# Performance work log

Hardware: AMD Instinct MI355X
Metric: run time of the kernel (lower is better)

Reference implementation:

```python
import jax, jax.numpy as jnp
import numpy as np

B, HH, WW, C = 16, 56, 56, 384
HEADS, WS, SHIFT, HID = 12, 7, 3, 1536
N = WS * WS
EPS = 1e-5


def _rel_pos_index(ws):
    coords = np.stack(np.meshgrid(np.arange(ws), np.arange(ws), indexing='ij'))  # (2, ws, ws)
    cf = coords.reshape(2, -1)
    rel = (cf[:, :, None] - cf[:, None, :]).transpose(1, 2, 0).copy()  # (N, N, 2)
    rel[:, :, 0] += ws - 1
    rel[:, :, 1] += ws - 1
    rel[:, :, 0] *= 2 * ws - 1
    return rel.sum(-1)  # (N, N) int


def _attn_mask(H, W, ws, shift):
    img = np.zeros((H, W))
    sl = (slice(0, -ws), slice(-ws, -shift), slice(-shift, None))
    cnt = 0
    for h in sl:
        for w in sl:
            img[h, w] = cnt
            cnt += 1
    mw = img.reshape(H // ws, ws, W // ws, ws).transpose(0, 2, 1, 3).reshape(-1, ws * ws)  # (nW, N)
    am = mw[:, None, :] - mw[:, :, None]
    return np.where(am != 0, -100.0, 0.0).astype(np.float32)  # (nW, N, N)

REL_IDX = jnp.asarray(_rel_pos_index(WS))
ATTN_MASK = jnp.asarray(_attn_mask(HH, WW, WS, SHIFT))


def _ln(x, w, b):
    m = x.mean(-1, keepdims=True)
    v = ((x - m) ** 2).mean(-1, keepdims=True)
    return (x - m) * jax.lax.rsqrt(v + EPS) * w + b


def _win_part(x, ws):
    b, h, w, c = x.shape
    x = x.reshape(b, h // ws, ws, w // ws, ws, c).transpose(0, 1, 3, 2, 4, 5)
    return x.reshape(-1, ws * ws, c)


def _win_rev(wins, ws, h, w):
    c = wins.shape[-1]
    b = wins.shape[0] // ((h // ws) * (w // ws))
    x = wins.reshape(b, h // ws, w // ws, ws, ws, c).transpose(0, 1, 3, 2, 4, 5)
    return x.reshape(b, h, w, c)


def setup_inputs() -> dict:
    key = jax.random.key(0)
    ks = jax.random.split(key, 12)
    s = lambda fan: 1.0 / np.sqrt(fan)
    return {
        'x': jax.random.normal(ks[0], (B, HH * WW, C), jnp.float32),
        'norm1_w': jnp.ones((C,), jnp.float32),
        'norm1_b': jnp.zeros((C,), jnp.float32),
        'qkv_w': jax.random.normal(ks[1], (3 * C, C), jnp.float32) * s(C),
        'qkv_b': jnp.zeros((3 * C,), jnp.float32),
        'bias_table': jax.random.normal(ks[2], ((2 * WS - 1) ** 2, HEADS), jnp.float32) * 0.02,
        'proj_w': jax.random.normal(ks[3], (C, C), jnp.float32) * s(C),
        'proj_b': jnp.zeros((C,), jnp.float32),
        'norm2_w': jnp.ones((C,), jnp.float32),
        'norm2_b': jnp.zeros((C,), jnp.float32),
        'mlp_w1': jax.random.normal(ks[4], (HID, C), jnp.float32) * s(C),
        'mlp_b1': jnp.zeros((HID,), jnp.float32),
        'mlp_w2': jax.random.normal(ks[5], (C, HID), jnp.float32) * s(HID),
        'mlp_b2': jnp.zeros((C,), jnp.float32),
        'H': HH,
        'W': WW,
    }


def reference(x, norm1_w, norm1_b, qkv_w, qkv_b, bias_table, proj_w, proj_b,
              norm2_w, norm2_b, mlp_w1, mlp_b1, mlp_w2, mlp_b2, H, W):
    b = x.shape[0]
    shortcut = x
    h = _ln(x, norm1_w, norm1_b).reshape(b, H, W, C)
    # cyclic shift (H, W divisible by WS -> no padding needed)
    h = jnp.roll(h, shift=(-SHIFT, -SHIFT), axis=(1, 2))
    xw = _win_part(h, WS)  # (b*nW, N, C)
    Bw = xw.shape[0]
    hd = C // HEADS
    qkv = xw @ qkv_w.T + qkv_b  # (Bw, N, 3C)
    qkv = qkv.reshape(Bw, N, 3, HEADS, hd).transpose(2, 0, 3, 1, 4)
    q, k, v = qkv[0], qkv[1], qkv[2]  # (Bw, heads, N, hd)
    attn = jnp.einsum('bhnd,bhmd->bhnm', q * (hd ** -0.5), k)
    rel_bias = bias_table[REL_IDX.reshape(-1)].reshape(N, N, HEADS).transpose(2, 0, 1)
    attn = attn + rel_bias[None]
    nW = ATTN_MASK.shape[0]
    attn = attn.reshape(Bw // nW, nW, HEADS, N, N) + ATTN_MASK[None, :, None]
    attn = jax.nn.softmax(attn.reshape(Bw, HEADS, N, N), axis=-1)
    out = jnp.einsum('bhnm,bhmd->bhnd', attn, v).transpose(0, 2, 1, 3).reshape(Bw, N, C)
    out = out @ proj_w.T + proj_b
    h = _win_rev(out, WS, H, W)
    h = jnp.roll(h, shift=(SHIFT, SHIFT), axis=(1, 2)).reshape(b, H * W, C)
    x = shortcut + h
    y = _ln(x, norm2_w, norm2_b)
    y = jax.nn.gelu(y @ mlp_w1.T + mlp_b1, approximate=False) @ mlp_w2.T + mlp_b2
    return x + y
```

## Files before the change

### kernel.cpp

```cpp
#include <hip/hip_runtime.h>

typedef unsigned short ushort_t;
typedef __attribute__((ext_vector_type(8))) short bf16x8;
typedef __attribute__((ext_vector_type(4))) float f32x4;

__device__ __forceinline__ float b2f(ushort_t u) {
    union { float f; unsigned int u32; } x; x.u32 = ((unsigned int)u) << 16; return x.f;
}
__device__ __forceinline__ ushort_t f2b(float f) {
    union { float f; unsigned int u; } x; x.f = f;
    unsigned int r = x.u + 0x7fffu + ((x.u >> 16) & 1u);
    return (ushort_t)(r >> 16);
}
__device__ __forceinline__ float ldin(const void* p, size_t i, int fp32) {
    return fp32 ? ((const float*)p)[i] : b2f(((const ushort_t*)p)[i]);
}
__device__ __forceinline__ void gl_lds16(const ushort_t* g, ushort_t* l) {
    __builtin_amdgcn_global_load_lds((const __attribute__((address_space(1))) unsigned int*)g,
                                     (__attribute__((address_space(3))) unsigned int*)l, 16, 0, 0);
}
__device__ __forceinline__ float gelu_f(float x) {
    float xx = x * x;
    float u  = x * (0.7978845608028654f + 0.0356774081363f * xx);
    float a  = __builtin_fabsf(u);
    float e2 = __expf(-2.0f * a);
    float t  = (1.0f - e2) * __builtin_amdgcn_rcpf(1.0f + e2);
    t = __builtin_copysignf(t, u);
    return 0.5f * x * (1.0f + t);
}

struct Cv { const void* s; ushort_t* d; int n; };
struct CvA { Cv a[13]; };
__global__ void convert_all(CvA c, int total) {
    int fp32 = (*(const unsigned int*)c.a[0].s == 0x3F800000u);
    for (int idx = blockIdx.x * blockDim.x + threadIdx.x; idx < total; idx += gridDim.x * blockDim.x) {
        int i = idx, k = 0;
        while (k < 12 && i >= c.a[k].n) { i -= c.a[k].n; ++k; }
        c.a[k].d[i] = fp32 ? f2b(((const float*)c.a[k].s)[i]) : ((const ushort_t*)c.a[k].s)[i];
    }
}

__global__ __launch_bounds__(256) void ln_kernel(const void* __restrict__ x,
                                                 const ushort_t* __restrict__ w,
                                                 const ushort_t* __restrict__ bvec,
                                                 ushort_t* __restrict__ out, int mode, int row_base,
                                                 const void* __restrict__ flagsrc)
{
    int wave = threadIdx.x >> 6, lane = threadIdx.x & 63;
    int lr = blockIdx.x * 4 + wave;
    int r = row_base + lr;
    int f32 = (mode == 1) ? 1 : (*(const unsigned int*)flagsrc == 0x3F800000u);
    long src;
    if (mode == 0) {
        int win = r / 49, pos = r % 49;
        int b = win >> 6, wy = (win >> 3) & 7, wx = win & 7;
        int py = pos / 7, px = pos - py * 7;
        int ys = wy * 7 + py + 3; if (ys >= 56) ys -= 56;
        int xs = wx * 7 + px + 3; if (xs >= 56) xs -= 56;
        src = (long)b * 3136 + ys * 56 + xs;
    } else {
        src = r;
    }
    float v[6];
    float s = 0.f, sq = 0.f;
#pragma unroll
    for (int j = 0; j < 6; ++j) {
        v[j] = ldin(x, src * 384 + lane + 64 * j, f32);
        s += v[j]; sq += v[j] * v[j];
    }
#pragma unroll
    for (int off = 32; off; off >>= 1) { s += __shfl_xor(s, off); sq += __shfl_xor(sq, off); }
    float mean = s * (1.f / 384.f);
    float var  = sq * (1.f / 384.f) - mean * mean;
    float rstd = rsqrtf(var + 1e-5f);
    ushort_t* op = out + (size_t)lr * 384;
#pragma unroll
    for (int j = 0; j < 6; ++j) {
        int c = lane + 64 * j;
        op[c] = f2b((v[j] - mean) * rstd * b2f(w[c]) + b2f(bvec[c]));
    }
}

__global__ __launch_bounds__(256) void attn_mfma(const ushort_t* __restrict__ qkv,
                                                 const ushort_t* __restrict__ bt,
                                                 ushort_t* __restrict__ out)
{
    __shared__ __align__(16) ushort_t Pb[4][64 * 72];
    __shared__ __align__(16) ushort_t Vb[4][32 * 72];
    int win = blockIdx.x;
    int t = threadIdx.x;
    int wave = t >> 6, lane = t & 63;
    int quad = lane >> 4, l16 = lane & 15;
    ushort_t* P  = Pb[wave];
    ushort_t* VT = Vb[wave];
    int wimg = win & 63;
    int wy = wimg >> 3, wx = wimg & 7;
    const float scale = 0.17677669529663687f;

    int rjv[4], cjv[4], gjv[4], cvalid[4];
#pragma unroll
    for (int jt = 0; jt < 4; ++jt) {
        int c = jt * 16 + l16;
        cvalid[jt] = (c < 49);
        int rj = c / 7, cj = c - rj * 7;
        rjv[jt] = rj; cjv[jt] = cj;
        int gjy = (wy == 7) ? (rj < 4 ? 1 : 2) : 0;
        int gjx = (wx == 7) ? (cj < 4 ? 1 : 2) : 0;
        gjv[jt] = gjy * 3 + gjx;
    }

    for (int hh = 0; hh < 3; ++hh) {
        int head = wave * 3 + hh;
        size_t base = (size_t)win * 49 * 1152 + (size_t)head * 32;

        bf16x8 qf[4], kf[4];
#pragma unroll
        for (int i = 0; i < 4; ++i) {
            int row = i * 16 + l16;
            bf16x8 z = {};
            qf[i] = z; kf[i] = z;
            if (row < 49) {
                qf[i] = *(const bf16x8*)(qkv + base + (size_t)row * 1152 + quad * 8);
                kf[i] = *(const bf16x8*)(qkv + base + (size_t)row * 1152 + 384 + quad * 8);
            }
        }
#pragma unroll
        for (int e = 0; e < 4; ++e) {
            int j = e * 16 + (lane >> 2);
            int db = (lane & 3) * 8;
            ushort_t buf[8] = {};
            if (j < 49) *(uint4*)buf = *(const uint4*)(qkv + base + (size_t)j * 1152 + 768 + db);
#pragma unroll
            for (int s = 0; s < 8; ++s) VT[(db + s) * 72 + j] = buf[s];
        }

        f32x4 Sv[4][4];
#pragma unroll
        for (int i = 0; i < 4; ++i)
#pragma unroll
            for (int j = 0; j < 4; ++j) {
                f32x4 z = {};
                Sv[i][j] = __builtin_amdgcn_mfma_f32_16x16x32_bf16(qf[i], kf[j], z, 0, 0, 0);
            }

#pragma unroll
        for (int it = 0; it < 4; ++it) {
#pragma unroll
            for (int r = 0; r < 4; ++r) {
                int m = it * 16 + quad * 4 + r;
                int ri = m / 7, ci = m - ri * 7;
                int giy = (wy == 7) ? (ri < 4 ? 1 : 2) : 0;
                int gix = (wx == 7) ? (ci < 4 ? 1 : 2) : 0;
                int gi = giy * 3 + gix;
                float vals[4];
                float vmax = -1e30f;
#pragma unroll
                for (int jt = 0; jt < 4; ++jt) {
                    float sv = -1e30f;
                    if (m < 49 && cvalid[jt]) {
                        int rel = (ri - rjv[jt] + 6) * 13 + (ci - cjv[jt] + 6);
                        sv = Sv[it][jt][r] * scale + b2f(bt[rel * 12 + head]);
                        if (gi != gjv[jt]) sv -= 100.f;
                    }
                    vals[jt] = sv;
                    vmax = fmaxf(vmax, sv);
                }
#pragma unroll
                for (int off = 1; off < 16; off <<= 1) vmax = fmaxf(vmax, __shfl_xor(vmax, off));
                float ssum = 0.f;
#pragma unroll
                for (int jt = 0; jt < 4; ++jt) { float e = __expf(vals[jt] - vmax); vals[jt] = e; ssum += e; }
#pragma unroll
                for (int off = 1; off < 16; off <<= 1) ssum += __shfl_xor(ssum, off);
                float inv = __builtin_amdgcn_rcpf(ssum);
#pragma unroll
                for (int jt = 0; jt < 4; ++jt) P[m * 72 + jt * 16 + l16] = f2b(vals[jt] * inv);
            }
        }

        f32x4 Ov[4][2] = {};
#pragma unroll
        for (int kk = 0; kk < 2; ++kk) {
            bf16x8 vb[2];
            vb[0] = *(const bf16x8*)&VT[(l16) * 72 + kk * 32 + quad * 8];
            vb[1] = *(const bf16x8*)&VT[(16 + l16) * 72 + kk * 32 + quad * 8];
#pragma unroll
            for (int mt = 0; mt < 4; ++mt) {
                bf16x8 pa = *(const bf16x8*)&P[(mt * 16 + l16) * 72 + kk * 32 + quad * 8];
                Ov[mt][0] = __builtin_amdgcn_mfma_f32_16x16x32_bf16(pa, vb[0], Ov[mt][0], 0, 0, 0);
                Ov[mt][1] = __builtin_amdgcn_mfma_f32_16x16x32_bf16(pa, vb[1], Ov[mt][1], 0, 0, 0);
            }
        }
#pragma unroll
        for (int mt = 0; mt < 4; ++mt)
#pragma unroll
            for (int r = 0; r < 4; ++r) {
                int m = mt * 16 + quad * 4 + r;
                if (m < 49) {
                    size_t orow = ((size_t)win * 49 + m) * 384 + (size_t)head * 32;
                    out[orow + l16]      = f2b(Ov[mt][0][r]);
                    out[orow + 16 + l16] = f2b(Ov[mt][1][r]);
                }
            }
    }
}

template <int EPI>
__global__ __launch_bounds__(512, 4) void gemm_k(const ushort_t* __restrict__ A,
                                                 const ushort_t* __restrict__ Bw,
                                                 const ushort_t* __restrict__ bias,
                                                 const void* __restrict__ residv,
                                                 void* __restrict__ outv,
                                                 int N, int K, int Mp, long rbase,
                                                 const void* __restrict__ flagsrc)
{
    __shared__ __align__(16) ushort_t lA[3][256 * 32];
    __shared__ __align__(16) ushort_t lB[3][128 * 32];

    unsigned gx = gridDim.x;
    unsigned nwg = gx * gridDim.y;
    unsigned lid = blockIdx.y * gx + blockIdx.x;
    unsigned xcd = lid & 7u, chunk_i = lid >> 3;
    unsigned q = nwg >> 3, r8 = nwg & 7u;
    unsigned logical = (xcd < r8 ? xcd * (q + 1) : r8 * (q + 1) + (xcd - r8) * q) + chunk_i;
    int m0 = (int)(logical / gx) * 256, n0 = (int)(logical % gx) * 128;

    int t = threadIdx.x;
    int wave = t >> 6, lane = t & 63;
    int quad = lane >> 4, l16 = lane & 15;
    int wrow = (wave >> 1) * 64, wcol = (wave & 1) * 64;
    f32x4 acc[4][4] = {};

    float bb[4];
#pragma unroll
    for (int j = 0; j < 4; ++j) bb[j] = b2f(bias[n0 + wcol + j * 16 + l16]);
    asm volatile("" :: "v"(bb[0]), "v"(bb[1]), "v"(bb[2]), "v"(bb[3]));

    const ushort_t* gp[3];
    ushort_t* lp[3];
    int lstr[3];
#pragma unroll
    for (int e = 0; e < 3; ++e) {
        int chunk = wave * 3 + e;
        int a = (chunk < 16);
        int trow = (a ? chunk * 16 : (chunk - 16) * 16) + (lane >> 2);
        int fsw = (trow >> 1) & 3;
        int scol = ((lane & 3) ^ fsw) * 8;
        int grow = a ? (m0 + trow) : (n0 + trow);
        if (a && grow >= Mp) grow = Mp - 1;
        gp[e] = (a ? A : Bw) + (size_t)grow * K + scol;
        lp[e] = a ? &lA[0][chunk * 512] : &lB[0][(chunk - 16) * 512];
        lstr[e] = a ? 256 * 32 : 128 * 32;
    }

    auto stage = [&](int buf, int k0) {
#pragma unroll
        for (int e = 0; e < 3; ++e)
            gl_lds16(gp[e] + k0, lp[e] + buf * lstr[e]);
    };

    int sl = (quad ^ ((l16 >> 1) & 3)) * 8;
    auto compute = [&](int buf) {
        bf16x8 af[4], bf[4];
#pragma unroll
        for (int i = 0; i < 4; ++i)
            af[i] = *(const bf16x8*)(&lA[buf][(wrow + i * 16 + l16) * 32 + sl]);
#pragma unroll
        for (int j = 0; j < 4; ++j)
            bf[j] = *(const bf16x8*)(&lB[buf][(wcol + j * 16 + l16) * 32 + sl]);
#pragma unroll
        for (int i = 0; i < 4; ++i)
#pragma unroll
            for (int j = 0; j < 4; ++j)
                acc[i][j] = __builtin_amdgcn_mfma_f32_16x16x32_bf16(af[i], bf[j], acc[i][j], 0, 0, 0);
    };

    int T = K >> 5;
    stage(0, 0);
    stage(1, 32);

    int cur = 0;
    for (int tt = 0; tt < T - 1; ++tt) {
        asm volatile("s_waitcnt vmcnt(3)" ::: "memory");
        __builtin_amdgcn_s_barrier();
        if (tt + 2 < T) stage(cur == 0 ? 2 : cur - 1, (tt + 2) * 32);
        compute(cur);
        cur = (cur == 2) ? 0 : cur + 1;
    }
    asm volatile("s_waitcnt vmcnt(0)" ::: "memory");
    __builtin_amdgcn_s_barrier();
    compute(cur);

    int rf32 = (EPI == 2) ? (*(const unsigned int*)flagsrc == 0x3F800000u) : 1;

#pragma unroll
    for (int i = 0; i < 4; ++i) {
#pragma unroll
        for (int rix = 0; rix < 4; ++rix) {
            int m = m0 + wrow + i * 16 + quad * 4 + rix;
            if (m >= Mp) continue;
            unsigned orow = 0;
            if (EPI == 2) {
                int mg = (int)rbase + m;
                int win = mg / 49, pos = mg - win * 49;
                int b = win >> 6, wy = (win >> 3) & 7, wx = win & 7;
                int py = pos / 7, px = pos - py * 7;
                int y = wy * 7 + py + 3; if (y >= 56) y -= 56;
                int x = wx * 7 + px + 3; if (x >= 56) x -= 56;
                orow = (unsigned)(b * 3136 + y * 56 + x);
            } else if (EPI == 3) {
                orow = (unsigned)(rbase + m);
            }
#pragma unroll
            for (int j = 0; j < 4; ++j) {
                int n = n0 + wcol + j * 16 + l16;
                float vv = acc[i][j][rix] + bb[j];
                if (EPI == 0) {
                    ((ushort_t*)outv)[(unsigned)m * (unsigned)N + (unsigned)n] = f2b(vv);
                } else if (EPI == 1) {
                    ((ushort_t*)outv)[(unsigned)m * (unsigned)N + (unsigned)n] = f2b(gelu_f(vv));
                } else {
                    float r = ldin(residv, (size_t)orow * 384 + n, rf32);
                    ((float*)outv)[(size_t)orow * 384 + n] = vv + r;
                }
            }
        }
    }
}

extern "C" void kernel_launch(void* const* d_in, const int* in_sizes, int n_in,
                              void* d_out, int out_size, void* d_ws, size_t ws_size,
                              hipStream_t stream)
{
    (void)in_sizes; (void)n_in; (void)out_size;
    char* ws = (char*)d_ws;
    size_t off = 0;
    auto alloc = [&](size_t bytes) { size_t p = off; off = (off + bytes + 255) & ~(size_t)255; return p; };

    size_t o_n1w  = alloc(384 * 2);
    size_t o_n1b  = alloc(384 * 2);
    size_t o_qw   = alloc(442368ull * 2);
    size_t o_qb   = alloc(1152 * 2);
    size_t o_bt   = alloc(2028 * 2);
    size_t o_pw   = alloc(147456ull * 2);
    size_t o_pb   = alloc(384 * 2);
    size_t o_n2w  = alloc(384 * 2);
    size_t o_n2b  = alloc(384 * 2);
    size_t o_w1   = alloc(589824ull * 2);
    size_t o_b1   = alloc(1536 * 2);
    size_t o_w2   = alloc(589824ull * 2);
    size_t o_b2   = alloc(384 * 2);

    size_t avail = (ws_size > off) ? ws_size - off : 0;
    int M_c;
    if      (avail >= (size_t)50176 * 3840 + 1024) M_c = 50176;
    else if (avail >= (size_t)12544 * 3840 + 1024) M_c = 12544;
    else                                            M_c = 6272;
    int nch = 50176 / M_c;
    size_t o_s1 = alloc((size_t)M_c * 768);
    size_t o_s2 = alloc((size_t)M_c * 3072);

    ushort_t* n1w  = (ushort_t*)(ws + o_n1w);
    ushort_t* n1b  = (ushort_t*)(ws + o_n1b);
    ushort_t* qw   = (ushort_t*)(ws + o_qw);
    ushort_t* qb   = (ushort_t*)(ws + o_qb);
    ushort_t* bt   = (ushort_t*)(ws + o_bt);
    ushort_t* pw   = (ushort_t*)(ws + o_pw);
    ushort_t* pb   = (ushort_t*)(ws + o_pb);
    ushort_t* n2w  = (ushort_t*)(ws + o_n2w);
    ushort_t* n2b  = (ushort_t*)(ws + o_n2b);
    ushort_t* w1   = (ushort_t*)(ws + o_w1);
    ushort_t* b1   = (ushort_t*)(ws + o_b1);
    ushort_t* w2   = (ushort_t*)(ws + o_w2);
    ushort_t* b2v  = (ushort_t*)(ws + o_b2);
    ushort_t* s1   = (ushort_t*)(ws + o_s1);
    ushort_t* s2   = (ushort_t*)(ws + o_s2);
    const void* x  = d_in[0];
    const void* fs = d_in[1];
    float* xmid    = (float*)d_out;

    CvA ca;
    ca.a[0]  = {d_in[1],  n1w, 384};
    ca.a[1]  = {d_in[2],  n1b, 384};
    ca.a[2]  = {d_in[3],  qw,  442368};
    ca.a[3]  = {d_in[4],  qb,  1152};
    ca.a[4]  = {d_in[5],  bt,  2028};
    ca.a[5]  = {d_in[6],  pw,  147456};
    ca.a[6]  = {d_in[7],  pb,  384};
    ca.a[7]  = {d_in[8],  n2w, 384};
    ca.a[8]  = {d_in[9],  n2b, 384};
    ca.a[9]  = {d_in[10], w1,  589824};
    ca.a[10] = {d_in[11], b1,  1536};
    ca.a[11] = {d_in[12], w2,  589824};
    ca.a[12] = {d_in[13], b2v, 384};
    convert_all<<<2048, 256, 0, stream>>>(ca, 1776492);

    for (int c = 0; c < nch; ++c) {
        int rb = c * M_c;
        int gy = (M_c + 255) / 256;
        ln_kernel<<<dim3(M_c / 4), dim3(256), 0, stream>>>(x, n1w, n1b, s1, 0, rb, fs);
        gemm_k<0><<<dim3(9, gy), dim3(512), 0, stream>>>(s1, qw, qb, nullptr, s2, 1152, 384, M_c, 0, fs);
        attn_mfma<<<dim3(M_c / 49), dim3(256), 0, stream>>>(s2, bt, s1);
        gemm_k<2><<<dim3(3, gy), dim3(512), 0, stream>>>(s1, pw, pb, x, xmid, 384, 384, M_c, rb, fs);
    }
    for (int c = 0; c < nch; ++c) {
        int rb = c * M_c;
        int gy = (M_c + 255) / 256;
        ln_kernel<<<dim3(M_c / 4), dim3(256), 0, stream>>>(xmid, n2w, n2b, s1, 1, rb, fs);
        gemm_k<1><<<dim3(12, gy), dim3(512), 0, stream>>>(s1, w1, b1, nullptr, s2, 1536, 384, M_c, 0, fs);
        gemm_k<3><<<dim3(3, gy), dim3(512), 0, stream>>>(s2, w2, b2v, xmid, (float*)d_out, 384, 1536, M_c, rb, fs);
    }
}
```

Baseline: 594.0 us.

## Vectorize LayerNorm loads/stores, raise MFMA wave priority, add intermediate chunk size

The LayerNorm kernel now gives each lane contiguous channel groups (4 plus 2). It loads them with float4/float2 or ushort4/ushort2 and stores packed bf16 pairs, where it used to do strided scalar accesses. The attention kernel wraps its MFMA loops in s_setprio so waves issuing matrix work get scheduling priority. A 25088-row chunk option is added for the MLP workspace when memory sits between the existing thresholds. The LayerNorm change reduces the number of memory instructions. The chunk option only takes effect for intermediate workspace sizes.

```diff
diff --git a/kernel.cpp b/kernel.cpp
--- a/kernel.cpp
+++ b/kernel.cpp
@@ -11,6 +11,9 @@
     union { float f; unsigned int u; } x; x.f = f;
     unsigned int r = x.u + 0x7fffu + ((x.u >> 16) & 1u);
     return (ushort_t)(r >> 16);
+}
+__device__ __forceinline__ unsigned pack2(float a, float b) {
+    return (unsigned)f2b(a) | ((unsigned)f2b(b) << 16);
 }
 __device__ __forceinline__ float ldin(const void* p, size_t i, int fp32) {
     return fp32 ? ((const float*)p)[i] : b2f(((const ushort_t*)p)[i]);
@@ -61,24 +64,39 @@
     } else {
         src = r;
     }
+    int c0 = lane * 4, c1 = 256 + lane * 2;
     float v[6];
+    if (f32) {
+        const float* rp = (const float*)x + src * 384;
+        float4 a = *(const float4*)(rp + c0);
+        float2 b = *(const float2*)(rp + c1);
+        v[0] = a.x; v[1] = a.y; v[2] = a.z; v[3] = a.w; v[4] = b.x; v[5] = b.y;
+    } else {
+        const ushort_t* rp = (const ushort_t*)x + src * 384;
+        ushort4 a = *(const ushort4*)(rp + c0);
+        ushort2 b = *(const ushort2*)(rp + c1);
+        v[0] = b2f(a.x); v[1] = b2f(a.y); v[2] = b2f(a.z); v[3] = b2f(a.w);
+        v[4] = b2f(b.x); v[5] = b2f(b.y);
+    }
     float s = 0.f, sq = 0.f;
 #pragma unroll
-    for (int j = 0; j < 6; ++j) {
-        v[j] = ldin(x, src * 384 + lane + 64 * j, f32);
-        s += v[j]; sq += v[j] * v[j];
-    }
+    for (int j = 0; j < 6; ++j) { s += v[j]; sq += v[j] * v[j]; }
 #pragma unroll
     for (int off = 32; off; off >>= 1) { s += __shfl_xor(s, off); sq += __shfl_xor(sq, off); }
     float mean = s * (1.f / 384.f);
     float var  = sq * (1.f / 384.f) - mean * mean;
     float rstd = rsqrtf(var + 1e-5f);
+    float o[6];
+    o[0] = (v[0] - mean) * rstd * b2f(w[c0])     + b2f(bvec[c0]);
+    o[1] = (v[1] - mean) * rstd * b2f(w[c0 + 1]) + b2f(bvec[c0 + 1]);
+    o[2] = (v[2] - mean) * rstd * b2f(w[c0 + 2]) + b2f(bvec[c0 + 2]);
+    o[3] = (v[3] - mean) * rstd * b2f(w[c0 + 3]) + b2f(bvec[c0 + 3]);
+    o[4] = (v[4] - mean) * rstd * b2f(w[c1])     + b2f(bvec[c1]);
+    o[5] = (v[5] - mean) * rstd * b2f(w[c1 + 1]) + b2f(bvec[c1 + 1]);
     ushort_t* op = out + (size_t)lr * 384;
-#pragma unroll
-    for (int j = 0; j < 6; ++j) {
-        int c = lane + 64 * j;
-        op[c] = f2b((v[j] - mean) * rstd * b2f(w[c]) + b2f(bvec[c]));
-    }
+    uint2 p01; p01.x = pack2(o[0], o[1]); p01.y = pack2(o[2], o[3]);
+    *(uint2*)(op + c0) = p01;
+    *(unsigned*)(op + c1) = pack2(o[4], o[5]);
 }
 
 __global__ __launch_bounds__(256) void attn_mfma(const ushort_t* __restrict__ qkv,
@@ -135,6 +153,7 @@
         }
 
         f32x4 Sv[4][4];
+        __builtin_amdgcn_s_setprio(1);
 #pragma unroll
         for (int i = 0; i < 4; ++i)
 #pragma unroll
@@ -142,6 +161,7 @@
                 f32x4 z = {};
                 Sv[i][j] = __builtin_amdgcn_mfma_f32_16x16x32_bf16(qf[i], kf[j], z, 0, 0, 0);
             }
+        __builtin_amdgcn_s_setprio(0);
 
 #pragma unroll
         for (int it = 0; it < 4; ++it) {
@@ -184,12 +204,14 @@
             bf16x8 vb[2];
             vb[0] = *(const bf16x8*)&VT[(l16) * 72 + kk * 32 + quad * 8];
             vb[1] = *(const bf16x8*)&VT[(16 + l16) * 72 + kk * 32 + quad * 8];
+            __builtin_amdgcn_s_setprio(1);
 #pragma unroll
             for (int mt = 0; mt < 4; ++mt) {
                 bf16x8 pa = *(const bf16x8*)&P[(mt * 16 + l16) * 72 + kk * 32 + quad * 8];
                 Ov[mt][0] = __builtin_amdgcn_mfma_f32_16x16x32_bf16(pa, vb[0], Ov[mt][0], 0, 0, 0);
                 Ov[mt][1] = __builtin_amdgcn_mfma_f32_16x16x32_bf16(pa, vb[1], Ov[mt][1], 0, 0, 0);
             }
+            __builtin_amdgcn_s_setprio(0);
         }
 #pragma unroll
         for (int mt = 0; mt < 4; ++mt)
@@ -354,6 +376,7 @@
     size_t avail = (ws_size > off) ? ws_size - off : 0;
     int M_c;
     if      (avail >= (size_t)50176 * 3840 + 1024) M_c = 50176;
+    else if (avail >= (size_t)25088 * 3840 + 1024) M_c = 25088;
     else if (avail >= (size_t)12544 * 3840 + 1024) M_c = 12544;
     else                                            M_c = 6272;
     int nch = 50176 / M_c;
```

Result: no change. 589.7 us (-0.7%).
